# Performance work log

Hardware: AMD Instinct MI355X
Metric: run time of the kernel (lower is better)

Reference implementation:

```python
import jax, jax.numpy as jnp
import numpy as np

H, D = 12, 128          # heads, head_dim
DIM = 1536              # vid_dim == txt_dim == H*D
EPS = 1e-6


def _rmsnorm(x, w):
    # RMSNorm over last dim (head_dim) with learnable scale
    var = jnp.mean(jnp.square(x), axis=-1, keepdims=True)
    return x * jax.lax.rsqrt(var + EPS) * w


def setup_inputs() -> dict:
    key = jax.random.key(0)
    ks = jax.random.split(key, 16)
    B, Lv, Lt = 2, 2 * 24 * 40, 128
    inner = H * D
    s = 0.02
    inp = {
        "vid": jax.random.normal(ks[0], (B * Lv, DIM), jnp.float32),
        "txt": jax.random.normal(ks[1], (B * Lt, DIM), jnp.float32),
        "Wqkv_vid": jax.random.normal(ks[2], (DIM, 3 * inner), jnp.float32) * s,
        "bqkv_vid": jnp.zeros((3 * inner,), jnp.float32),
        "Wqkv_txt": jax.random.normal(ks[3], (DIM, 3 * inner), jnp.float32) * s,
        "bqkv_txt": jnp.zeros((3 * inner,), jnp.float32),
        "nq_vid": jnp.ones((D,), jnp.float32),
        "nk_vid": jnp.ones((D,), jnp.float32),
        "nq_txt": jnp.ones((D,), jnp.float32),
        "nk_txt": jnp.ones((D,), jnp.float32),
        "Wout_vid": jax.random.normal(ks[4], (inner, DIM), jnp.float32) * s,
        "bout_vid": jnp.zeros((DIM,), jnp.float32),
        "Wout_txt": jax.random.normal(ks[5], (inner, DIM), jnp.float32) * s,
        "bout_txt": jnp.zeros((DIM,), jnp.float32),
        # static per-sample shapes (numpy => usable as Python ints under jit)
        "vid_shape": np.array([[2, 24, 40], [2, 24, 40]], np.int64),
        "txt_shape": np.array([[128], [128]], np.int64),
    }
    return inp


def reference(vid, txt, Wqkv_vid, bqkv_vid, Wqkv_txt, bqkv_txt,
              nq_vid, nk_vid, nq_txt, nk_txt,
              Wout_vid, bout_vid, Wout_txt, bout_txt,
              vid_shape, txt_shape):
    B = vid_shape.shape[0]
    Lv = int(np.prod(vid_shape[0]))   # equal lengths across batch
    Lt = int(txt_shape[0, 0])

    # fused QKV projections (separate weights for vid/txt, shared_weights=False)
    vid_qkv = (vid @ Wqkv_vid + bqkv_vid).reshape(-1, 3, H, D)
    txt_qkv = (txt @ Wqkv_txt + bqkv_txt).reshape(-1, 3, H, D)
    vq, vk, vv = vid_qkv[:, 0], vid_qkv[:, 1], vid_qkv[:, 2]
    tq, tk, tv = txt_qkv[:, 0], txt_qkv[:, 1], txt_qkv[:, 2]

    # QK-norm (per-modality RMSNorm over head_dim)
    vq, tq = _rmsnorm(vq, nq_vid), _rmsnorm(tq, nq_txt)
    vk, tk = _rmsnorm(vk, nk_vid), _rmsnorm(tk, nk_txt)

    # multimodal packing: per sample, vid tokens then txt tokens (cu_seqlens over vid_len+txt_len)
    def pack(v, t):
        v = v.reshape(B, Lv, H, D)
        t = t.reshape(B, Lt, H, D)
        return jnp.concatenate([v, t], axis=1)  # [B, Lv+Lt, H, D]

    q = pack(vq, tq).astype(jnp.bfloat16)
    k = pack(vk, tk).astype(jnp.bfloat16)
    v = pack(vv, tv).astype(jnp.bfloat16)

    scale = 1.0 / np.sqrt(D)
    scores = jnp.einsum('blhd,bmhd->bhlm', q, k,
                        preferred_element_type=jnp.float32) * scale
    probs = jax.nn.softmax(scores, axis=-1)
    out = jnp.einsum('bhlm,bmhd->blhd', probs.astype(jnp.bfloat16), v,
                     preferred_element_type=jnp.float32).astype(vid.dtype)

    # unconcat + head merge
    out = out.reshape(B, Lv + Lt, H * D)
    vid_out = out[:, :Lv].reshape(B * Lv, H * D)
    txt_out = out[:, Lv:].reshape(B * Lt, H * D)

    vid_out = vid_out @ Wout_vid + bout_vid
    txt_out = txt_out @ Wout_txt + bout_txt
    return (vid_out, txt_out)
```

## Files before the change

### kernel.cpp

```cpp
#include <hip/hip_runtime.h>
#include <hip/hip_bf16.h>
#include <stdint.h>

typedef __attribute__((ext_vector_type(8))) short  short8;
typedef __attribute__((ext_vector_type(4))) float  f32x4;
typedef __attribute__((ext_vector_type(4))) unsigned int uint4v;
typedef __attribute__((ext_vector_type(4))) unsigned short ushort4v;

#define MFMA16(a,b,c) __builtin_amdgcn_mfma_f32_16x16x32_bf16((a),(b),(c),0,0,0)

#define AS1 __attribute__((address_space(1)))
#define AS3 __attribute__((address_space(3)))
static __device__ __forceinline__ void gload16(void* lds, const void* g) {
  __builtin_amdgcn_global_load_lds((AS1 const void*)g, (AS3 void*)lds, 16, 0, 0);
}

static __device__ __forceinline__ unsigned short f2bf(float x) {
  unsigned int u = __float_as_uint(x);
  u += 0x7fffu + ((u >> 16) & 1u);
  return (unsigned short)(u >> 16);
}
static __device__ __forceinline__ float bf2f(unsigned short h) {
  return __uint_as_float(((unsigned int)h) << 16);
}

#define HDS   12
#define DD    128
#define DIMK  1536
#define NIN   4608
#define LV    1920
#define LT    128
#define LL    2048
#define BB    2
#define MV    3840
#define MT    256
#define MTOT  4096
#define QSC   (0.08838834764831845f * 1.4426950408889634f)

__global__ __launch_bounds__(256) void split_x(const float* __restrict__ vid,
                                               const float* __restrict__ txt,
                                               unsigned short* __restrict__ xhi) {
  size_t i = ((size_t)blockIdx.x * 256 + threadIdx.x) * 4;
  const size_t NV = (size_t)MV * DIMK;
  const float* src = (i < NV) ? (vid + i) : (txt + (i - NV));
  f32x4 v = *(const f32x4*)src;
  ushort4v hv;
#pragma unroll
  for (int j = 0; j < 4; ++j) hv[j] = f2bf(v[j]);
  *(ushort4v*)(xhi + i) = hv;
}

__global__ __launch_bounds__(256) void transpose_cast(const float* __restrict__ W,
                                                      unsigned short* __restrict__ Thi,
                                                      int K, int N) {
  __shared__ float tile[32][33];
  const int tx = threadIdx.x & 31, ty = threadIdx.x >> 5;
  const int k0 = blockIdx.y * 32, n0 = blockIdx.x * 32;
#pragma unroll
  for (int i = 0; i < 32; i += 8)
    tile[ty + i][tx] = W[(size_t)(k0 + ty + i) * N + n0 + tx];
  __syncthreads();
#pragma unroll
  for (int i = 0; i < 32; i += 8)
    Thi[(size_t)(n0 + ty + i) * K + k0 + tx] = f2bf(tile[tx][ty + i]);
}

__global__ __launch_bounds__(256) void vt_transpose(const unsigned short* __restrict__ v,
                                                    unsigned short* __restrict__ vtb) {
  __shared__ unsigned short tile[32][33];
  const int tx = threadIdx.x & 31, ty = threadIdx.x >> 5;
  const int bh = blockIdx.z;
  const int l0 = blockIdx.x * 32, d0 = blockIdx.y * 32;
  const size_t base = (size_t)bh * LL * DD;
#pragma unroll
  for (int i = 0; i < 32; i += 8)
    tile[ty + i][tx] = v[base + (size_t)(l0 + ty + i) * DD + d0 + tx];
  __syncthreads();
#pragma unroll
  for (int i = 0; i < 32; i += 8)
    vtb[base + (size_t)(d0 + ty + i) * LL + l0 + tx] = tile[tx][ty + i];
}

__device__ __forceinline__ void bf16_mainloop256(
    const unsigned short* __restrict__ Ahi, const unsigned short* __restrict__ Bhi,
    int m0, int n0,
    uint4v* __restrict__ sA, uint4v* __restrict__ sB,
    f32x4 (&acc)[4][4]) {
  const int t = threadIdx.x;
  const int lane = t & 63;
  const int w = t >> 6;
  const int wm = w >> 1, wn = w & 1;
  const int lr = lane & 15, lg = lane >> 4;
  const int ra = t >> 1, ca = (t & 1) * 2;
  const int rb = t >> 2, cb = t & 3;
  const size_t arow = (size_t)(m0 + ra) * DIMK + ca * 8;
  const size_t brow = (size_t)(n0 + rb) * DIMK + cb * 8;
  const int sa0 = ca * 256 + ra, sa1 = (ca + 1) * 256 + ra;
  const int sb0 = cb * 128 + rb;
  const int fA = lg * 256 + wm * 64 + lr;
  const int fB = lg * 128 + wn * 64 + lr;

  uint4v aA0 = *(const uint4v*)(Ahi + arow);
  uint4v aA1 = *(const uint4v*)(Ahi + arow + 8);
  uint4v bA0 = *(const uint4v*)(Bhi + brow);
  uint4v aB0 = *(const uint4v*)(Ahi + arow + 32);
  uint4v aB1 = *(const uint4v*)(Ahi + arow + 40);
  uint4v bB0 = *(const uint4v*)(Bhi + brow + 32);

  for (int k0 = 0; k0 < DIMK; k0 += 64) {
    sA[sa0] = aA0; sA[sa1] = aA1; sB[sb0] = bA0;
    if (k0 + 64 < DIMK) {
      aA0 = *(const uint4v*)(Ahi + arow + k0 + 64);
      aA1 = *(const uint4v*)(Ahi + arow + k0 + 72);
      bA0 = *(const uint4v*)(Bhi + brow + k0 + 64);
    }
    __syncthreads();
    {
      short8 ah[4], bh[4];
#pragma unroll
      for (int i = 0; i < 4; ++i) {
        ah[i] = *(const short8*)&sA[fA + i * 16];
        bh[i] = *(const short8*)&sB[fB + i * 16];
      }
#pragma unroll
      for (int mi = 0; mi < 4; ++mi)
#pragma unroll
        for (int ni = 0; ni < 4; ++ni)
          acc[mi][ni] = MFMA16(ah[mi], bh[ni], acc[mi][ni]);
    }
    sA[1024 + sa0] = aB0; sA[1024 + sa1] = aB1; sB[512 + sb0] = bB0;
    if (k0 + 96 < DIMK) {
      aB0 = *(const uint4v*)(Ahi + arow + k0 + 96);
      aB1 = *(const uint4v*)(Ahi + arow + k0 + 104);
      bB0 = *(const uint4v*)(Bhi + brow + k0 + 96);
    }
    __syncthreads();
    {
      short8 ah[4], bh[4];
#pragma unroll
      for (int i = 0; i < 4; ++i) {
        ah[i] = *(const short8*)&sA[1024 + fA + i * 16];
        bh[i] = *(const short8*)&sB[512 + fB + i * 16];
      }
#pragma unroll
      for (int mi = 0; mi < 4; ++mi)
#pragma unroll
        for (int ni = 0; ni < 4; ++ni)
          acc[mi][ni] = MFMA16(ah[mi], bh[ni], acc[mi][ni]);
    }
  }
}

__global__ __launch_bounds__(512) void gemm_qkv(
    const unsigned short* __restrict__ Xhi,
    const unsigned short* __restrict__ WvH, const unsigned short* __restrict__ WtH,
    const float* __restrict__ bias_v, const float* __restrict__ bias_t,
    const float* __restrict__ nq_v, const float* __restrict__ nk_v,
    const float* __restrict__ nq_t, const float* __restrict__ nk_t,
    unsigned short* __restrict__ qb, unsigned short* __restrict__ kb,
    unsigned short* __restrict__ vb) {
  __shared__ uint4v sA[2048], sB[1024];
  __shared__ float rowsq[2][256];
  const int t = threadIdx.x;
  const int lane = t & 63;
  const int w = t >> 6;
  const int wm = w >> 1, wn = w & 1;
  const int lr = lane & 15, lg = lane >> 4;
  const int bid = blockIdx.x;
  const int xcd = bid & 7, ii = bid >> 3;
  const int mt = xcd * 2 + (ii & 1), nt = ii >> 1;
  const int m0 = mt * 256, n0 = nt * 128;
  const bool istxt = (m0 >= MV);
  const unsigned short* WThi = istxt ? WtH : WvH;
  const float* bias = istxt ? bias_t : bias_v;
  const int Lmod = istxt ? LT : LV;
  const int loff = istxt ? LV : 0;
  const int mbase = istxt ? MV : 0;

  f32x4 acc[4][4];
#pragma unroll
  for (int mi = 0; mi < 4; ++mi)
#pragma unroll
    for (int ni = 0; ni < 4; ++ni) acc[mi][ni] = (f32x4){0.f, 0.f, 0.f, 0.f};

  bf16_mainloop256(Xhi, WThi, m0, n0, sA, sB, acc);

  const int s  = n0 / DIMK;
  const int hh = (n0 % DIMK) / DD;
#pragma unroll
  for (int ni = 0; ni < 4; ++ni) {
    float bv = bias[n0 + wn * 64 + ni * 16 + lr];
#pragma unroll
    for (int mi = 0; mi < 4; ++mi)
#pragma unroll
      for (int r = 0; r < 4; ++r) acc[mi][ni][r] += bv;
  }
  if (s < 2) {
    __syncthreads();
#pragma unroll
    for (int mi = 0; mi < 4; ++mi)
#pragma unroll
      for (int r = 0; r < 4; ++r) {
        float p = 0.f;
#pragma unroll
        for (int ni = 0; ni < 4; ++ni) p += acc[mi][ni][r] * acc[mi][ni][r];
        p += __shfl_xor(p, 1); p += __shfl_xor(p, 2);
        p += __shfl_xor(p, 4); p += __shfl_xor(p, 8);
        if (lr == 0) rowsq[wn][wm * 64 + mi * 16 + lg * 4 + r] = p;
      }
    __syncthreads();
    const float* nw = (s == 0) ? (istxt ? nq_t : nq_v) : (istxt ? nk_t : nk_v);
    const float post = (s == 0) ? QSC : 1.0f;
    float nwv[4];
#pragma unroll
    for (int ni = 0; ni < 4; ++ni) nwv[ni] = nw[wn * 64 + ni * 16 + lr] * post;
#pragma unroll
    for (int mi = 0; mi < 4; ++mi)
#pragma unroll
      for (int r = 0; r < 4; ++r) {
        int row = wm * 64 + mi * 16 + lg * 4 + r;
        float a = (rowsq[0][row] + rowsq[1][row]) * (1.f / 128.f) + 1e-6f;
        float x = rsqrtf(a);
        x = x * (1.5f - 0.5f * a * x * x);
#pragma unroll
        for (int ni = 0; ni < 4; ++ni) acc[mi][ni][r] *= x * nwv[ni];
      }
  }
  unsigned short* dst = (s == 0) ? qb : ((s == 1) ? kb : vb);
#pragma unroll
  for (int mi = 0; mi < 4; ++mi)
#pragma unroll
    for (int r = 0; r < 4; ++r) {
      int mrow = m0 + wm * 64 + mi * 16 + lg * 4 + r - mbase;
      int bidx = (mrow >= Lmod) ? 1 : 0;
      int l = loff + mrow - bidx * Lmod;
      size_t rb2 = ((size_t)(bidx * HDS + hh) * LL + l) * DD;
#pragma unroll
      for (int ni = 0; ni < 4; ++ni) {
        int d = wn * 64 + ni * 16 + lr;
        dst[rb2 + d] = f2bf(acc[mi][ni][r]);
      }
    }
}

__global__ __launch_bounds__(256) void attn_kernel(
    const unsigned short* __restrict__ qb, const unsigned short* __restrict__ kb,
    const unsigned short* __restrict__ vt,
    unsigned short* __restrict__ aohi) {
  const int t = threadIdx.x;
  const int lane = t & 63, w = t >> 6;
  const int lr = lane & 15, lg = lane >> 4;
  const int bid = blockIdx.x;
  const int xcd = bid & 7, ii = bid >> 3;
  const int bh = xcd * 3 + (ii >> 5);
  const int qt = ii & 31;
  const int q0 = (qt * 4 + w) * 16;
  const size_t base = (size_t)bh * LL * DD;

  __shared__ __align__(16) unsigned short Kbuf[2][32 * 128];
  __shared__ __align__(16) unsigned short Vbuf[2][128 * 32];
  __shared__ __align__(16) unsigned short P[4][16 * 40];

  const char* kglob = (const char*)(kb + base);
  const char* vglob = (const char*)(vt + base);

  const int  srcK  = (t * 16) ^ (((t >> 4) & 7) << 4);
  const size_t vs0 = (size_t)(t >> 2) * (LL * 2) +
                     (((t & 3) ^ ((t >> 2) & 3)) << 4);
  const size_t vs1 = vs0 + (size_t)64 * (LL * 2);
  char* kd0 = (char*)Kbuf + w * 1024;
  char* kd1 = kd0 + 4096;
  char* vd0 = (char*)Vbuf + w * 1024;
  char* vd1 = vd0 + 4096;

  int akr[2][4];
#pragma unroll
  for (int h = 0; h < 2; ++h) {
    const int rr = 2 * lr + h;
#pragma unroll
    for (int ks = 0; ks < 4; ++ks)
      akr[h][ks] = rr * 256 + ((ks * 64 + lg * 16) ^ ((rr & 7) << 4));
  }
  const int av0 = lr * 64 + ((lg ^ (lr & 3)) << 4);
  char* pwr = (char*)P + w * 1280 + lg * 320 + lr * 4;
  const char* prd = (const char*)P + w * 1280 + lr * 80 + lg * 16;
  const char* KBp = (const char*)Kbuf;
  const char* VBp = (const char*)Vbuf;

  short8 qf[4];
#pragma unroll
  for (int ks = 0; ks < 4; ++ks)
    qf[ks] = *(const short8*)(qb + base + (size_t)(q0 + lr) * DD + ks * 32 + lg * 8);

  f32x4 o[8];
#pragma unroll
  for (int i = 0; i < 8; ++i) o[i] = (f32x4){0.f, 0.f, 0.f, 0.f};
  float Z[4] = {0.f, 0.f, 0.f, 0.f};

  const char* gkp = kglob;
  const char* gvp = vglob;
  gload16(kd0, gkp + srcK);
  gload16(kd1, gkp + 4096 + srcK);
  gload16(vd0, gvp + vs0);
  gload16(vd1, gvp + vs1);
  __syncthreads();

#pragma unroll 2
  for (int kt = 0; kt < LL / 32; ++kt) {
    const int cur = kt & 1;
    const int cb = cur * 8192, nb = (cur ^ 1) * 8192;
    if (kt + 1 < LL / 32) {
      gload16(kd0 + nb, gkp + 8192 + srcK);
      gload16(kd1 + nb, gkp + 8192 + 4096 + srcK);
      gload16(vd0 + nb, gvp + 64 + vs0);
      gload16(vd1 + nb, gvp + 64 + vs1);
    }
    f32x4 s0a = (f32x4){0.f, 0.f, 0.f, 0.f}, s0b = (f32x4){0.f, 0.f, 0.f, 0.f};
    f32x4 s1a = (f32x4){0.f, 0.f, 0.f, 0.f}, s1b = (f32x4){0.f, 0.f, 0.f, 0.f};
#pragma unroll
    for (int ks = 0; ks < 4; ++ks) {
      short8 k0f = *(const short8*)(KBp + cb + akr[0][ks]);
      short8 k1f = *(const short8*)(KBp + cb + akr[1][ks]);
      if (ks < 2) { s0a = MFMA16(qf[ks], k0f, s0a); s1a = MFMA16(qf[ks], k1f, s1a); }
      else        { s0b = MFMA16(qf[ks], k0f, s0b); s1b = MFMA16(qf[ks], k1f, s1b); }
    }
#pragma unroll
    for (int r = 0; r < 4; ++r) {
      float p0, p1;
      float sa = s0a[r] + s0b[r];
      float sb = s1a[r] + s1b[r];
      asm("v_exp_f32 %0, %1" : "=v"(p0) : "v"(sa));
      asm("v_exp_f32 %0, %1" : "=v"(p1) : "v"(sb));
      Z[r] += p0 + p1;
      unsigned int u;
      asm("v_cvt_pk_bf16_f32 %0, %1, %2" : "=v"(u) : "v"(p0), "v"(p1));
      *(unsigned int*)(pwr + r * 80) = u;
    }
    short8 pa = *(const short8*)prd;
#pragma unroll
    for (int df = 0; df < 8; ++df) {
      short8 vf = *(const short8*)(VBp + cb + df * 1024 + av0);
      o[df] = MFMA16(pa, vf, o[df]);
    }
    __syncthreads();
    gkp += 8192; gvp += 64;
  }

  float invZ[4];
#pragma unroll
  for (int r = 0; r < 4; ++r) {
    Z[r] += __shfl_xor(Z[r], 1); Z[r] += __shfl_xor(Z[r], 2);
    Z[r] += __shfl_xor(Z[r], 4); Z[r] += __shfl_xor(Z[r], 8);
    invZ[r] = 1.0f / Z[r];
  }

  const int b = bh / HDS, h = bh % HDS;
#pragma unroll
  for (int df = 0; df < 8; ++df)
#pragma unroll
    for (int r = 0; r < 4; ++r) {
      int l = q0 + lg * 4 + r;
      size_t row = (l < LV) ? ((size_t)b * LV + l) : ((size_t)MV + b * LT + (l - LV));
      int col = h * DD + df * 16 + lr;
      aohi[row * DIMK + col] = f2bf(o[df][r] * invZ[r]);
    }
}

__device__ __forceinline__ void bf16_mainloop128(
    const unsigned short* __restrict__ Ahi, const unsigned short* __restrict__ Bhi,
    int m0, int n0,
    uint4v* __restrict__ sA, uint4v* __restrict__ sB,
    f32x4 (&acc)[4][4]) {
  const int t = threadIdx.x;
  const int lane = t & 63;
  const int w = t >> 6;
  const int wm = w >> 1, wn = w & 1;
  const int lr = lane & 15, lg = lane >> 4;
  const int sr = t >> 1;
  const int sc = (t & 1) * 2;
  const size_t arow = (size_t)(m0 + sr) * DIMK + sc * 8;
  const size_t brow = (size_t)(n0 + sr) * DIMK + sc * 8;
  const int slot0 = sc * 128 + sr, slot1 = (sc + 1) * 128 + sr;
  const int fA = lg * 128 + wm * 64 + lr;
  const int fB = lg * 128 + wn * 64 + lr;

  uint4v aA0 = *(const uint4v*)(Ahi + arow);
  uint4v aA1 = *(const uint4v*)(Ahi + arow + 8);
  uint4v bA0 = *(const uint4v*)(Bhi + brow);
  uint4v bA1 = *(const uint4v*)(Bhi + brow + 8);
  uint4v aB0 = *(const uint4v*)(Ahi + arow + 32);
  uint4v aB1 = *(const uint4v*)(Ahi + arow + 40);
  uint4v bB0 = *(const uint4v*)(Bhi + brow + 32);
  uint4v bB1 = *(const uint4v*)(Bhi + brow + 40);

  for (int k0 = 0; k0 < DIMK; k0 += 64) {
    sA[slot0] = aA0; sA[slot1] = aA1;
    sB[slot0] = bA0; sB[slot1] = bA1;
    if (k0 + 64 < DIMK) {
      aA0 = *(const uint4v*)(Ahi + arow + k0 + 64);
      aA1 = *(const uint4v*)(Ahi + arow + k0 + 72);
      bA0 = *(const uint4v*)(Bhi + brow + k0 + 64);
      bA1 = *(const uint4v*)(Bhi + brow + k0 + 72);
    }
    __syncthreads();
    {
      short8 ah[4], bh[4];
#pragma unroll
      for (int i = 0; i < 4; ++i) {
        ah[i] = *(const short8*)&sA[fA + i * 16];
        bh[i] = *(const short8*)&sB[fB + i * 16];
      }
#pragma unroll
      for (int mi = 0; mi < 4; ++mi)
#pragma unroll
        for (int ni = 0; ni < 4; ++ni)
          acc[mi][ni] = MFMA16(ah[mi], bh[ni], acc[mi][ni]);
    }
    sA[512 + slot0] = aB0; sA[512 + slot1] = aB1;
    sB[512 + slot0] = bB0; sB[512 + slot1] = bB1;
    if (k0 + 96 < DIMK) {
      aB0 = *(const uint4v*)(Ahi + arow + k0 + 96);
      aB1 = *(const uint4v*)(Ahi + arow + k0 + 104);
      bB0 = *(const uint4v*)(Bhi + brow + k0 + 96);
      bB1 = *(const uint4v*)(Bhi + brow + k0 + 104);
    }
    __syncthreads();
    {
      short8 ah[4], bh[4];
#pragma unroll
      for (int i = 0; i < 4; ++i) {
        ah[i] = *(const short8*)&sA[512 + fA + i * 16];
        bh[i] = *(const short8*)&sB[512 + fB + i * 16];
      }
#pragma unroll
      for (int mi = 0; mi < 4; ++mi)
#pragma unroll
        for (int ni = 0; ni < 4; ++ni)
          acc[mi][ni] = MFMA16(ah[mi], bh[ni], acc[mi][ni]);
    }
  }
}

__global__ __launch_bounds__(256) void gemm_out(
    const unsigned short* __restrict__ Ahi,
    const unsigned short* __restrict__ WvH, const unsigned short* __restrict__ WtH,
    const float* __restrict__ bias_v, const float* __restrict__ bias_t,
    float* __restrict__ out) {
  __shared__ uint4v sA[1024], sB[1024];
  const int t = threadIdx.x;
  const int lane = t & 63;
  const int w = t >> 6;
  const int wm = w >> 1, wn = w & 1;
  const int lr = lane & 15, lg = lane >> 4;
  const int bid = blockIdx.x;
  const int xcd = bid & 7, ii = bid >> 3;
  const int mt = xcd * 4 + (ii & 3), nt = ii >> 2;
  const int m0 = mt * 128, n0 = nt * 128;
  const bool istxt = (m0 >= MV);
  const unsigned short* WThi = istxt ? WtH : WvH;
  const float* bias = istxt ? bias_t : bias_v;

  f32x4 acc[4][4];
#pragma unroll
  for (int mi = 0; mi < 4; ++mi)
#pragma unroll
    for (int ni = 0; ni < 4; ++ni) acc[mi][ni] = (f32x4){0.f, 0.f, 0.f, 0.f};

  bf16_mainloop128(Ahi, WThi, m0, n0, sA, sB, acc);

#pragma unroll
  for (int ni = 0; ni < 4; ++ni) {
    float bv = bias[n0 + wn * 64 + ni * 16 + lr];
#pragma unroll
    for (int mi = 0; mi < 4; ++mi)
#pragma unroll
      for (int r = 0; r < 4; ++r) {
        size_t row = (size_t)(m0 + wm * 64 + mi * 16 + lg * 4 + r);
        out[row * DIMK + n0 + wn * 64 + ni * 16 + lr] = acc[mi][ni][r] + bv;
      }
  }
}

extern "C" void kernel_launch(void* const* d_in, const int* in_sizes, int n_in,
                              void* d_out, int out_size, void* d_ws, size_t ws_size,
                              hipStream_t stream) {
  (void)in_sizes; (void)n_in; (void)out_size; (void)ws_size;
  const float* vid      = (const float*)d_in[0];
  const float* txt      = (const float*)d_in[1];
  const float* Wqkv_vid = (const float*)d_in[2];
  const float* bqkv_vid = (const float*)d_in[3];
  const float* Wqkv_txt = (const float*)d_in[4];
  const float* bqkv_txt = (const float*)d_in[5];
  const float* nq_vid   = (const float*)d_in[6];
  const float* nk_vid   = (const float*)d_in[7];
  const float* nq_txt   = (const float*)d_in[8];
  const float* nk_txt   = (const float*)d_in[9];
  const float* Wout_vid = (const float*)d_in[10];
  const float* bout_vid = (const float*)d_in[11];
  const float* Wout_txt = (const float*)d_in[12];
  const float* bout_txt = (const float*)d_in[13];
  float* out = (float*)d_out;

  char* ws = (char*)d_ws;
  size_t off = 0;
  auto alloc = [&](size_t bytes) { char* p = ws + off; off += (bytes + 255) & ~(size_t)255; return p; };

  const size_t SZ_X    = (size_t)MTOT * DIMK * 2;
  const size_t SZ_WQKV = (size_t)NIN * DIMK * 2;
  const size_t SZ_WOUT = (size_t)DIMK * DIMK * 2;
  const size_t SZ_QKVB = (size_t)BB * HDS * LL * DD * 2;

  unsigned short* Xhi   = (unsigned short*)alloc(SZ_X);
  unsigned short* WTqvH = (unsigned short*)alloc(SZ_WQKV);
  unsigned short* WTqtH = (unsigned short*)alloc(SZ_WQKV);
  unsigned short* WTovH = (unsigned short*)alloc(SZ_WOUT);
  unsigned short* WTotH = (unsigned short*)alloc(SZ_WOUT);
  unsigned short* QB    = (unsigned short*)alloc(SZ_QKVB);
  unsigned short* KB    = (unsigned short*)alloc(SZ_QKVB);
  unsigned short* VB    = (unsigned short*)alloc(SZ_QKVB);
  unsigned short* VT    = WTqvH;
  unsigned short* AOhi  = Xhi;

  split_x<<<dim3((MTOT * DIMK) / (256 * 4)), dim3(256), 0, stream>>>(vid, txt, Xhi);
  transpose_cast<<<dim3(NIN / 32, DIMK / 32), dim3(256), 0, stream>>>(Wqkv_vid, WTqvH, DIMK, NIN);
  transpose_cast<<<dim3(NIN / 32, DIMK / 32), dim3(256), 0, stream>>>(Wqkv_txt, WTqtH, DIMK, NIN);
  transpose_cast<<<dim3(DIMK / 32, DIMK / 32), dim3(256), 0, stream>>>(Wout_vid, WTovH, DIMK, DIMK);
  transpose_cast<<<dim3(DIMK / 32, DIMK / 32), dim3(256), 0, stream>>>(Wout_txt, WTotH, DIMK, DIMK);
  gemm_qkv<<<dim3(576), dim3(512), 0, stream>>>(
      Xhi, WTqvH, WTqtH, bqkv_vid, bqkv_txt,
      nq_vid, nk_vid, nq_txt, nk_txt, QB, KB, VB);
  vt_transpose<<<dim3(LL / 32, DD / 32, BB * HDS), dim3(256), 0, stream>>>(VB, VT);
  attn_kernel<<<dim3(768), dim3(256), 0, stream>>>(QB, KB, VT, AOhi);
  gemm_out<<<dim3(384), dim3(256), 0, stream>>>(
      AOhi, WTovH, WTotH, bout_vid, bout_txt, out);
}
```

Measured before the change: 231.0 us.

## Fuse input bf16 cast and V transpose into QKV GEMM, merge weight casts

Drops the separate split_x conversion kernel: the QKV GEMM now loads fp32 activations directly and packs them to bf16 in registers before staging to LDS. The V-transpose kernel is also removed; the s==2 epilogue stages V tiles in LDS and writes them transposed straight into the VT layout. The weight transpose-casts are merged pairwise into two launches using blockIdx.z. The aim is fewer launches and less HBM round-tripping, at the cost of doubled fp32 A-operand load traffic inside the GEMM mainloop, which also moves from k-step 64 to 32 with more barriers.

New measurement: 237.9 us. 3.0% more time.

```diff
diff --git a/kernel.cpp b/kernel.cpp
--- a/kernel.cpp
+++ b/kernel.cpp
@@ -20,8 +20,10 @@
   u += 0x7fffu + ((u >> 16) & 1u);
   return (unsigned short)(u >> 16);
 }
-static __device__ __forceinline__ float bf2f(unsigned short h) {
-  return __uint_as_float(((unsigned int)h) << 16);
+static __device__ __forceinline__ unsigned int pkbf(float a, float b) {
+  unsigned int u;
+  asm("v_cvt_pk_bf16_f32 %0, %1, %2" : "=v"(u) : "v"(a), "v"(b));
+  return u;
 }
 
 #define HDS   12
@@ -37,23 +39,14 @@
 #define MTOT  4096
 #define QSC   (0.08838834764831845f * 1.4426950408889634f)
 
-__global__ __launch_bounds__(256) void split_x(const float* __restrict__ vid,
-                                               const float* __restrict__ txt,
-                                               unsigned short* __restrict__ xhi) {
-  size_t i = ((size_t)blockIdx.x * 256 + threadIdx.x) * 4;
-  const size_t NV = (size_t)MV * DIMK;
-  const float* src = (i < NV) ? (vid + i) : (txt + (i - NV));
-  f32x4 v = *(const f32x4*)src;
-  ushort4v hv;
-#pragma unroll
-  for (int j = 0; j < 4; ++j) hv[j] = f2bf(v[j]);
-  *(ushort4v*)(xhi + i) = hv;
-}
-
-__global__ __launch_bounds__(256) void transpose_cast(const float* __restrict__ W,
-                                                      unsigned short* __restrict__ Thi,
-                                                      int K, int N) {
+__global__ __launch_bounds__(256) void transpose_cast2(const float* __restrict__ W0,
+                                                       unsigned short* __restrict__ T0,
+                                                       const float* __restrict__ W1,
+                                                       unsigned short* __restrict__ T1,
+                                                       int K, int N) {
   __shared__ float tile[32][33];
+  const float* W = blockIdx.z ? W1 : W0;
+  unsigned short* T = blockIdx.z ? T1 : T0;
   const int tx = threadIdx.x & 31, ty = threadIdx.x >> 5;
   const int k0 = blockIdx.y * 32, n0 = blockIdx.x * 32;
 #pragma unroll
@@ -62,105 +55,23 @@
   __syncthreads();
 #pragma unroll
   for (int i = 0; i < 32; i += 8)
-    Thi[(size_t)(n0 + ty + i) * K + k0 + tx] = f2bf(tile[tx][ty + i]);
-}
-
-__global__ __launch_bounds__(256) void vt_transpose(const unsigned short* __restrict__ v,
-                                                    unsigned short* __restrict__ vtb) {
-  __shared__ unsigned short tile[32][33];
-  const int tx = threadIdx.x & 31, ty = threadIdx.x >> 5;
-  const int bh = blockIdx.z;
-  const int l0 = blockIdx.x * 32, d0 = blockIdx.y * 32;
-  const size_t base = (size_t)bh * LL * DD;
-#pragma unroll
-  for (int i = 0; i < 32; i += 8)
-    tile[ty + i][tx] = v[base + (size_t)(l0 + ty + i) * DD + d0 + tx];
-  __syncthreads();
-#pragma unroll
-  for (int i = 0; i < 32; i += 8)
-    vtb[base + (size_t)(d0 + ty + i) * LL + l0 + tx] = tile[tx][ty + i];
-}
-
-__device__ __forceinline__ void bf16_mainloop256(
-    const unsigned short* __restrict__ Ahi, const unsigned short* __restrict__ Bhi,
-    int m0, int n0,
-    uint4v* __restrict__ sA, uint4v* __restrict__ sB,
-    f32x4 (&acc)[4][4]) {
-  const int t = threadIdx.x;
-  const int lane = t & 63;
-  const int w = t >> 6;
-  const int wm = w >> 1, wn = w & 1;
-  const int lr = lane & 15, lg = lane >> 4;
-  const int ra = t >> 1, ca = (t & 1) * 2;
-  const int rb = t >> 2, cb = t & 3;
-  const size_t arow = (size_t)(m0 + ra) * DIMK + ca * 8;
-  const size_t brow = (size_t)(n0 + rb) * DIMK + cb * 8;
-  const int sa0 = ca * 256 + ra, sa1 = (ca + 1) * 256 + ra;
-  const int sb0 = cb * 128 + rb;
-  const int fA = lg * 256 + wm * 64 + lr;
-  const int fB = lg * 128 + wn * 64 + lr;
-
-  uint4v aA0 = *(const uint4v*)(Ahi + arow);
-  uint4v aA1 = *(const uint4v*)(Ahi + arow + 8);
-  uint4v bA0 = *(const uint4v*)(Bhi + brow);
-  uint4v aB0 = *(const uint4v*)(Ahi + arow + 32);
-  uint4v aB1 = *(const uint4v*)(Ahi + arow + 40);
-  uint4v bB0 = *(const uint4v*)(Bhi + brow + 32);
-
-  for (int k0 = 0; k0 < DIMK; k0 += 64) {
-    sA[sa0] = aA0; sA[sa1] = aA1; sB[sb0] = bA0;
-    if (k0 + 64 < DIMK) {
-      aA0 = *(const uint4v*)(Ahi + arow + k0 + 64);
-      aA1 = *(const uint4v*)(Ahi + arow + k0 + 72);
-      bA0 = *(const uint4v*)(Bhi + brow + k0 + 64);
-    }
-    __syncthreads();
-    {
-      short8 ah[4], bh[4];
-#pragma unroll
-      for (int i = 0; i < 4; ++i) {
-        ah[i] = *(const short8*)&sA[fA + i * 16];
-        bh[i] = *(const short8*)&sB[fB + i * 16];
-      }
-#pragma unroll
-      for (int mi = 0; mi < 4; ++mi)
-#pragma unroll
-        for (int ni = 0; ni < 4; ++ni)
-          acc[mi][ni] = MFMA16(ah[mi], bh[ni], acc[mi][ni]);
-    }
-    sA[1024 + sa0] = aB0; sA[1024 + sa1] = aB1; sB[512 + sb0] = bB0;
-    if (k0 + 96 < DIMK) {
-      aB0 = *(const uint4v*)(Ahi + arow + k0 + 96);
-      aB1 = *(const uint4v*)(Ahi + arow + k0 + 104);
-      bB0 = *(const uint4v*)(Bhi + brow + k0 + 96);
-    }
-    __syncthreads();
-    {
-      short8 ah[4], bh[4];
-#pragma unroll
-      for (int i = 0; i < 4; ++i) {
-        ah[i] = *(const short8*)&sA[1024 + fA + i * 16];
-        bh[i] = *(const short8*)&sB[512 + fB + i * 16];
-      }
-#pragma unroll
-      for (int mi = 0; mi < 4; ++mi)
-#pragma unroll
-        for (int ni = 0; ni < 4; ++ni)
-          acc[mi][ni] = MFMA16(ah[mi], bh[ni], acc[mi][ni]);
-    }
-  }
+    T[(size_t)(n0 + ty + i) * K + k0 + tx] = f2bf(tile[tx][ty + i]);
 }
 
 __global__ __launch_bounds__(512) void gemm_qkv(
-    const unsigned short* __restrict__ Xhi,
+    const float* __restrict__ vidf, const float* __restrict__ txtf,
     const unsigned short* __restrict__ WvH, const unsigned short* __restrict__ WtH,
     const float* __restrict__ bias_v, const float* __restrict__ bias_t,
     const float* __restrict__ nq_v, const float* __restrict__ nk_v,
     const float* __restrict__ nq_t, const float* __restrict__ nk_t,
     unsigned short* __restrict__ qb, unsigned short* __restrict__ kb,
-    unsigned short* __restrict__ vb) {
-  __shared__ uint4v sA[2048], sB[1024];
-  __shared__ float rowsq[2][256];
+    unsigned short* __restrict__ vt) {
+  __shared__ __align__(16) char smem[51200];
+  uint4v* sA = (uint4v*)smem;
+  uint4v* sB = (uint4v*)(smem + 32768);
+  float*  rowsq = (float*)(smem + 49152);
+  unsigned short* stg = (unsigned short*)smem;
+
   const int t = threadIdx.x;
   const int lane = t & 63;
   const int w = t >> 6;
@@ -176,6 +87,7 @@
   const int Lmod = istxt ? LT : LV;
   const int loff = istxt ? LV : 0;
   const int mbase = istxt ? MV : 0;
+  const float* Xf = (istxt ? txtf : vidf) + (size_t)(m0 - mbase) * DIMK;
 
   f32x4 acc[4][4];
 #pragma unroll
@@ -183,7 +95,53 @@
 #pragma unroll
     for (int ni = 0; ni < 4; ++ni) acc[mi][ni] = (f32x4){0.f, 0.f, 0.f, 0.f};
 
-  bf16_mainloop256(Xhi, WThi, m0, n0, sA, sB, acc);
+  {
+    const int ra = t >> 1, ca = (t & 1) * 2;
+    const int rb = t >> 2, cb = t & 3;
+    const size_t arowf = (size_t)ra * DIMK + ca * 8;
+    const size_t brow  = (size_t)(n0 + rb) * DIMK + cb * 8;
+    const int sa0 = ca * 256 + ra, sa1 = (ca + 1) * 256 + ra;
+    const int sb0 = cb * 128 + rb;
+    const int fA = lg * 256 + wm * 64 + lr;
+    const int fB = lg * 128 + wn * 64 + lr;
+
+    f32x4 fa0 = *(const f32x4*)(Xf + arowf);
+    f32x4 fa1 = *(const f32x4*)(Xf + arowf + 4);
+    f32x4 fa2 = *(const f32x4*)(Xf + arowf + 8);
+    f32x4 fa3 = *(const f32x4*)(Xf + arowf + 12);
+    uint4v vb0 = *(const uint4v*)(WThi + brow);
+
+    int cur = 0;
+    for (int k0 = 0; k0 < DIMK; k0 += 32) {
+      const int ha = cur * 1024, hb = cur * 512;
+      uint4v va0 = (uint4v){pkbf(fa0[0], fa0[1]), pkbf(fa0[2], fa0[3]),
+                            pkbf(fa1[0], fa1[1]), pkbf(fa1[2], fa1[3])};
+      uint4v va1 = (uint4v){pkbf(fa2[0], fa2[1]), pkbf(fa2[2], fa2[3]),
+                            pkbf(fa3[0], fa3[1]), pkbf(fa3[2], fa3[3])};
+      sA[ha + sa0] = va0; sA[ha + sa1] = va1;
+      sB[hb + sb0] = vb0;
+      if (k0 + 32 < DIMK) {
+        fa0 = *(const f32x4*)(Xf + arowf + k0 + 32);
+        fa1 = *(const f32x4*)(Xf + arowf + k0 + 36);
+        fa2 = *(const f32x4*)(Xf + arowf + k0 + 40);
+        fa3 = *(const f32x4*)(Xf + arowf + k0 + 44);
+        vb0 = *(const uint4v*)(WThi + brow + k0 + 32);
+      }
+      __syncthreads();
+      short8 ah[4], bh[4];
+#pragma unroll
+      for (int i = 0; i < 4; ++i) {
+        ah[i] = *(const short8*)&sA[ha + fA + i * 16];
+        bh[i] = *(const short8*)&sB[hb + fB + i * 16];
+      }
+#pragma unroll
+      for (int mi = 0; mi < 4; ++mi)
+#pragma unroll
+        for (int ni = 0; ni < 4; ++ni)
+          acc[mi][ni] = MFMA16(ah[mi], bh[ni], acc[mi][ni]);
+      cur ^= 1;
+    }
+  }
 
   const int s  = n0 / DIMK;
   const int hh = (n0 % DIMK) / DD;
@@ -195,20 +153,56 @@
 #pragma unroll
       for (int r = 0; r < 4; ++r) acc[mi][ni][r] += bv;
   }
-  if (s < 2) {
-    __syncthreads();
-#pragma unroll
-    for (int mi = 0; mi < 4; ++mi)
-#pragma unroll
-      for (int r = 0; r < 4; ++r) {
-        float p = 0.f;
-#pragma unroll
-        for (int ni = 0; ni < 4; ++ni) p += acc[mi][ni][r] * acc[mi][ni][r];
-        p += __shfl_xor(p, 1); p += __shfl_xor(p, 2);
-        p += __shfl_xor(p, 4); p += __shfl_xor(p, 8);
-        if (lr == 0) rowsq[wn][wm * 64 + mi * 16 + lg * 4 + r] = p;
-      }
-    __syncthreads();
+
+  if (s == 2) {
+    const int dcol = wn * 64;
+#pragma unroll
+    for (int h = 0; h < 2; ++h) {
+      __syncthreads();
+      if ((wm >> 1) == h) {
+#pragma unroll
+        for (int mi = 0; mi < 4; ++mi)
+#pragma unroll
+          for (int r = 0; r < 4; ++r) {
+            int lloc = (wm & 1) * 64 + mi * 16 + lg * 4 + r;
+#pragma unroll
+            for (int ni = 0; ni < 4; ++ni)
+              stg[lloc * 137 + dcol + ni * 16 + lr] = f2bf(acc[mi][ni][r]);
+          }
+      }
+      __syncthreads();
+      const int lc = t & 15, dd0 = t >> 4;
+      int gr = m0 + h * 128 + lc * 8 - mbase;
+      int bidx = (gr >= Lmod) ? 1 : 0;
+      int l = loff + gr - bidx * Lmod;
+      size_t vbase = (size_t)(bidx * HDS + hh) * DD * LL;
+#pragma unroll
+      for (int p = 0; p < 4; ++p) {
+        int dd = p * 32 + dd0;
+        short8 vv;
+#pragma unroll
+        for (int j = 0; j < 8; ++j)
+          vv[j] = (short)stg[(lc * 8 + j) * 137 + dd];
+        *(short8*)(vt + vbase + (size_t)dd * LL + l) = vv;
+      }
+    }
+    return;
+  }
+
+  __syncthreads();
+#pragma unroll
+  for (int mi = 0; mi < 4; ++mi)
+#pragma unroll
+    for (int r = 0; r < 4; ++r) {
+      float p = 0.f;
+#pragma unroll
+      for (int ni = 0; ni < 4; ++ni) p += acc[mi][ni][r] * acc[mi][ni][r];
+      p += __shfl_xor(p, 1); p += __shfl_xor(p, 2);
+      p += __shfl_xor(p, 4); p += __shfl_xor(p, 8);
+      if (lr == 0) rowsq[wn * 256 + wm * 64 + mi * 16 + lg * 4 + r] = p;
+    }
+  __syncthreads();
+  {
     const float* nw = (s == 0) ? (istxt ? nq_t : nq_v) : (istxt ? nk_t : nk_v);
     const float post = (s == 0) ? QSC : 1.0f;
     float nwv[4];
@@ -219,14 +213,14 @@
 #pragma unroll
       for (int r = 0; r < 4; ++r) {
         int row = wm * 64 + mi * 16 + lg * 4 + r;
-        float a = (rowsq[0][row] + rowsq[1][row]) * (1.f / 128.f) + 1e-6f;
+        float a = (rowsq[row] + rowsq[256 + row]) * (1.f / 128.f) + 1e-6f;
         float x = rsqrtf(a);
         x = x * (1.5f - 0.5f * a * x * x);
 #pragma unroll
         for (int ni = 0; ni < 4; ++ni) acc[mi][ni][r] *= x * nwv[ni];
       }
   }
-  unsigned short* dst = (s == 0) ? qb : ((s == 1) ? kb : vb);
+  unsigned short* dst = (s == 0) ? qb : kb;
 #pragma unroll
   for (int mi = 0; mi < 4; ++mi)
 #pragma unroll
@@ -505,31 +499,27 @@
   size_t off = 0;
   auto alloc = [&](size_t bytes) { char* p = ws + off; off += (bytes + 255) & ~(size_t)255; return p; };
 
-  const size_t SZ_X    = (size_t)MTOT * DIMK * 2;
   const size_t SZ_WQKV = (size_t)NIN * DIMK * 2;
   const size_t SZ_WOUT = (size_t)DIMK * DIMK * 2;
   const size_t SZ_QKVB = (size_t)BB * HDS * LL * DD * 2;
-
-  unsigned short* Xhi   = (unsigned short*)alloc(SZ_X);
+  const size_t SZ_AO   = (size_t)MTOT * DIMK * 2;
+
   unsigned short* WTqvH = (unsigned short*)alloc(SZ_WQKV);
   unsigned short* WTqtH = (unsigned short*)alloc(SZ_WQKV);
   unsigned short* WTovH = (unsigned short*)alloc(SZ_WOUT);
   unsigned short* WTotH = (unsigned short*)alloc(SZ_WOUT);
   unsigned short* QB    = (unsigned short*)alloc(SZ_QKVB);
   unsigned short* KB    = (unsigned short*)alloc(SZ_QKVB);
-  unsigned short* VB    = (unsigned short*)alloc(SZ_QKVB);
-  unsigned short* VT    = WTqvH;
-  unsigned short* AOhi  = Xhi;
-
-  split_x<<<dim3((MTOT * DIMK) / (256 * 4)), dim3(256), 0, stream>>>(vid, txt, Xhi);
-  transpose_cast<<<dim3(NIN / 32, DIMK / 32), dim3(256), 0, stream>>>(Wqkv_vid, WTqvH, DIMK, NIN);
-  transpose_cast<<<dim3(NIN / 32, DIMK / 32), dim3(256), 0, stream>>>(Wqkv_txt, WTqtH, DIMK, NIN);
-  transpose_cast<<<dim3(DIMK / 32, DIMK / 32), dim3(256), 0, stream>>>(Wout_vid, WTovH, DIMK, DIMK);
-  transpose_cast<<<dim3(DIMK / 32, DIMK / 32), dim3(256), 0, stream>>>(Wout_txt, WTotH, DIMK, DIMK);
+  unsigned short* VT    = (unsigned short*)alloc(SZ_QKVB);
+  unsigned short* AOhi  = (unsigned short*)alloc(SZ_AO);
+
+  transpose_cast2<<<dim3(NIN / 32, DIMK / 32, 2), dim3(256), 0, stream>>>(
+      Wqkv_vid, WTqvH, Wqkv_txt, WTqtH, DIMK, NIN);
+  transpose_cast2<<<dim3(DIMK / 32, DIMK / 32, 2), dim3(256), 0, stream>>>(
+      Wout_vid, WTovH, Wout_txt, WTotH, DIMK, DIMK);
   gemm_qkv<<<dim3(576), dim3(512), 0, stream>>>(
-      Xhi, WTqvH, WTqtH, bqkv_vid, bqkv_txt,
-      nq_vid, nk_vid, nq_txt, nk_txt, QB, KB, VB);
-  vt_transpose<<<dim3(LL / 32, DD / 32, BB * HDS), dim3(256), 0, stream>>>(VB, VT);
+      vid, txt, WTqvH, WTqtH, bqkv_vid, bqkv_txt,
+      nq_vid, nk_vid, nq_txt, nk_txt, QB, KB, VT);
   attn_kernel<<<dim3(768), dim3(256), 0, stream>>>(QB, KB, VT, AOhi);
   gemm_out<<<dim3(384), dim3(256), 0, stream>>>(
       AOhi, WTovH, WTotH, bout_vid, bout_txt, out);
```
